# Kernel optimization log

Hardware: AMD Instinct MI355X
Metric: run time of the kernel (lower is better)

## Reference

```python
import jax, jax.numpy as jnp
import numpy as np

N_NODES = 50000
N_EDGES = 800000
IN_F = 96
HID = 64
N_CLS = 32


def setup_inputs() -> dict:
    key = jax.random.key(0)
    k1, k2, k3, k4 = jax.random.split(key, 4)
    x = jax.random.normal(k1, (N_NODES, IN_F), dtype=jnp.float32)
    edge_index = jax.random.randint(k2, (2, N_EDGES), 0, N_NODES, dtype=jnp.int64)
    # xavier_uniform init for weights, zeros for bias
    lim1 = float(np.sqrt(6.0 / (IN_F + HID)))
    lim2 = float(np.sqrt(6.0 / (HID + N_CLS)))
    W1 = jax.random.uniform(k3, (IN_F, HID), minval=-lim1, maxval=lim1, dtype=jnp.float32)
    W2 = jax.random.uniform(k4, (HID, N_CLS), minval=-lim2, maxval=lim2, dtype=jnp.float32)
    b1 = jnp.zeros((HID,), dtype=jnp.float32)
    b2 = jnp.zeros((N_CLS,), dtype=jnp.float32)
    return {"x": x, "edge_index": edge_index, "W1": W1, "b1": b1, "W2": W2, "b2": b2}


def _ghost_conv(h, src, dst, W, b, num_nodes):
    # gather neighbor feats per edge, per-edge matmul, scatter-add, bias
    msg = h[src] @ W                                   # [E, out]
    agg = jax.ops.segment_sum(msg, dst, num_segments=num_nodes)  # [N, out]
    return agg + b


def reference(x, edge_index, W1, b1, W2, b2):
    src, dst = edge_index[0], edge_index[1]
    n = x.shape[0]
    h = jax.nn.relu(_ghost_conv(x, src, dst, W1, b1, n))
    # F.dropout(training=False) is identity in eval mode
    out = _ghost_conv(h, src, dst, W2, b2, n)
    return jax.nn.log_softmax(out, axis=1)
```

## Files before the change

kernel.cpp:

```cpp
#include <hip/hip_runtime.h>
#include <hip/hip_bf16.h>
#include <hip/hip_fp8.h>

typedef __attribute__((ext_vector_type(8))) short bf16x8;
typedef __attribute__((ext_vector_type(4))) float f32x4;
typedef __attribute__((ext_vector_type(2))) float f32x2;

#define NBLK 256
#define NBINS_PAD 800
#define BCAP 2048
#define W1LD 104
#define HLD 72

__device__ inline unsigned short f2bf(float f) {
    unsigned u = __float_as_uint(f);
    return (unsigned short)((u + 0x7fffu + ((u >> 16) & 1u)) >> 16);
}
__device__ inline unsigned pack2(float a, float b) {
    return (unsigned)f2bf(a) | ((unsigned)f2bf(b) << 16);
}
__device__ inline float blo(unsigned u) { return __uint_as_float(u << 16); }
__device__ inline float bhi(unsigned u) { return __uint_as_float(u & 0xffff0000u); }

__device__ inline void acc8(float* a, uint4 v) {
    a[0] += blo(v.x); a[1] += bhi(v.x);
    a[2] += blo(v.y); a[3] += bhi(v.y);
    a[4] += blo(v.z); a[5] += bhi(v.z);
    a[6] += blo(v.w); a[7] += bhi(v.w);
}

__device__ inline void accf8x4(float* a, unsigned u) {
    f32x2 lo = __builtin_amdgcn_cvt_pk_f32_fp8((int)u, false);
    f32x2 hi = __builtin_amdgcn_cvt_pk_f32_fp8((int)u, true);
    a[0] += lo.x; a[1] += lo.y; a[2] += hi.x; a[3] += hi.y;
}
__device__ inline void accf8(float* a, uint4 v) {
    accf8x4(a, v.x); accf8x4(a + 4, v.y); accf8x4(a + 8, v.z); accf8x4(a + 12, v.w);
}

__global__ __launch_bounds__(256) void fused_hist_gemm1(
        const int* __restrict__ ei, int* __restrict__ counts, int E, int chunk, int nb,
        const float* __restrict__ W1, const float* __restrict__ W2,
        unsigned short* __restrict__ w2t,
        const float* __restrict__ X,
        unsigned char* __restrict__ y1f8, int Mtiles) {
    __shared__ int hist[NBINS_PAD];
    __shared__ unsigned short w1l[64 * W1LD];
    int b = blockIdx.x, t = threadIdx.x;
    if (b < NBLK) {
        for (int i = t; i < NBINS_PAD; i += 256) hist[i] = 0;
        __syncthreads();
        int e0 = b * chunk;
        int n = E - e0; if (n > chunk) n = chunk; if (n < 0) n = 0;
        for (int i = t; i < n; i += 256) atomicAdd(&hist[ei[E + e0 + i] >> 6], 1);
        __syncthreads();
        for (int j = t; j < nb; j += 256) counts[j * NBLK + b] = hist[j];
        return;
    }
    if (b == NBLK) {
        for (int idx = t; idx < 64 * 32; idx += 256) {
            int n = idx / 64, k = idx - n * 64;
            w2t[idx] = f2bf(W2[k * 32 + n]);
        }
        return;
    }
    for (int idx = t; idx < 96 * 64; idx += 256) {
        int n = idx / 96, k = idx - n * 96;
        w1l[n * W1LD + k] = f2bf(W1[k * 64 + n]);
    }
    __syncthreads();
    int wave = (b - NBLK - 1) * 4 + (t >> 6);
    if (wave >= Mtiles) return;
    int lane = t & 63;
    int l15 = lane & 15, quad = lane >> 4;
    const float* arow = X + (long)(wave * 16 + l15) * 96 + quad * 8;
    f32x4 acc[4] = {{0,0,0,0},{0,0,0,0},{0,0,0,0},{0,0,0,0}};
#pragma unroll
    for (int tt = 0; tt < 3; ++tt) {
        float4 p0 = *(const float4*)(arow + tt * 32);
        float4 p1 = *(const float4*)(arow + tt * 32 + 4);
        union { bf16x8 v; unsigned u[4]; } a;
        a.u[0] = pack2(p0.x, p0.y); a.u[1] = pack2(p0.z, p0.w);
        a.u[2] = pack2(p1.x, p1.y); a.u[3] = pack2(p1.z, p1.w);
#pragma unroll
        for (int nt = 0; nt < 4; ++nt) {
            bf16x8 bfr = *(const bf16x8*)(w1l + (nt * 16 + l15) * W1LD + tt * 32 + quad * 8);
            acc[nt] = __builtin_amdgcn_mfma_f32_16x16x32_bf16(a.v, bfr, acc[nt], 0, 0, 0);
        }
    }
    int mbase = wave * 16 + quad * 4;
#pragma unroll
    for (int nt = 0; nt < 4; ++nt) {
        int col = nt * 16 + l15;
        int pk = __builtin_amdgcn_cvt_pk_fp8_f32(acc[nt][0], acc[nt][1], 0, false);
        pk = __builtin_amdgcn_cvt_pk_fp8_f32(acc[nt][2], acc[nt][3], pk, true);
#pragma unroll
        for (int r = 0; r < 4; ++r)
            y1f8[(long)(mbase + r) * 64 + col] = (unsigned char)((pk >> (8 * r)) & 0xff);
    }
}

__global__ __launch_bounds__(256) void rowscan(int* __restrict__ counts,
                                               int* __restrict__ btot, int nb) {
    int w = (blockIdx.x * 256 + threadIdx.x) >> 6;
    int lane = threadIdx.x & 63;
    if (w >= nb) return;
    int* row = counts + (size_t)w * NBLK;
    int c0 = row[lane * 4], c1 = row[lane * 4 + 1];
    int c2 = row[lane * 4 + 2], c3 = row[lane * 4 + 3];
    int sum = c0 + c1 + c2 + c3;
    int s = sum;
#pragma unroll
    for (int o = 1; o < 64; o <<= 1) {
        int tt = __shfl_up(s, o);
        if (lane >= o) s += tt;
    }
    int run = s - sum;
    row[lane * 4] = run;     run += c0;
    row[lane * 4 + 1] = run; run += c1;
    row[lane * 4 + 2] = run; run += c2;
    row[lane * 4 + 3] = run;
    if (lane == 63) btot[w] = s;
}

__global__ __launch_bounds__(256) void blk_place(const int* __restrict__ ei,
                                                 const int* __restrict__ counts,
                                                 unsigned* __restrict__ pairs,
                                                 int E, int chunk, int nb) {
    __shared__ int cur[NBINS_PAD];
    int b = blockIdx.x, t = threadIdx.x;
    for (int j = t; j < nb; j += 256) cur[j] = (j << 11) + counts[j * NBLK + b];
    __syncthreads();
    int e0 = b * chunk;
    int n = E - e0; if (n > chunk) n = chunk; if (n < 0) n = 0;
    for (int i = t; i < n; i += 256) {
        int s = ei[e0 + i], d = ei[E + e0 + i];
        int j = d >> 6;
        int pos = atomicAdd(&cur[j], 1);
        if (pos < ((j + 1) << 11))
            pairs[pos] = (unsigned)s | ((unsigned)(d & 63) << 16);
    }
}

__global__ __launch_bounds__(256) void bucket_fused(
        const unsigned* __restrict__ pairs, const int* __restrict__ btot,
        const uint4* __restrict__ y1f8,
        const float* __restrict__ b1, const unsigned short* __restrict__ w2t,
        int2* __restrict__ noderange, int* __restrict__ srcs,
        unsigned short* __restrict__ y2, int N) {
    __shared__ unsigned spk[BCAP];
    __shared__ int lsrc[BCAP];
    __shared__ int cnt64[64], cur64[64], rs[64], re[64];
    __shared__ unsigned short htile[64 * HLD];
    int b = blockIdx.x, t = threadIdx.x;
    int base = b << 11;
    int cnt = btot[b]; if (cnt > BCAP) cnt = BCAP;
    if (t < 64) cnt64[t] = 0;
    __syncthreads();
    for (int i = t; i < cnt; i += 256) {
        unsigned p = pairs[base + i];
        spk[i] = p;
        atomicAdd(&cnt64[(p >> 16) & 63], 1);
    }
    __syncthreads();
    if (t < 64) {
        int v = cnt64[t], x = v;
#pragma unroll
        for (int o = 1; o < 64; o <<= 1) {
            int y = __shfl_up(x, o);
            if (t >= o) x += y;
        }
        int excl = x - v;
        cur64[t] = excl;
        rs[t] = excl;
        re[t] = excl + v;
        int node = b * 64 + t;
        if (node < N) noderange[node] = make_int2(base + excl, base + excl + v);
    }
    __syncthreads();
    for (int i = t; i < cnt; i += 256) {
        unsigned p = spk[i];
        int pos = atomicAdd(&cur64[(p >> 16) & 63], 1);
        lsrc[pos] = (int)(p & 0xffffu);
    }
    __syncthreads();
    for (int i = t; i < cnt; i += 256) srcs[base + i] = lsrc[i];

    int dl = t >> 2, q = t & 3;
    int s0 = rs[dl], s1 = re[dl];
    float a[16];
#pragma unroll
    for (int i = 0; i < 16; ++i) a[i] = 0.f;
    const uint4* ybase = y1f8 + q;
    int e = s0;
    for (; e + 8 <= s1; e += 8) {
        uint4 u0 = ybase[(long)lsrc[e] * 4],     u1 = ybase[(long)lsrc[e + 1] * 4];
        uint4 u2 = ybase[(long)lsrc[e + 2] * 4], u3 = ybase[(long)lsrc[e + 3] * 4];
        uint4 u4 = ybase[(long)lsrc[e + 4] * 4], u5 = ybase[(long)lsrc[e + 5] * 4];
        uint4 u6 = ybase[(long)lsrc[e + 6] * 4], u7 = ybase[(long)lsrc[e + 7] * 4];
        accf8(a, u0); accf8(a, u1); accf8(a, u2); accf8(a, u3);
        accf8(a, u4); accf8(a, u5); accf8(a, u6); accf8(a, u7);
    }
    for (; e < s1; ++e) accf8(a, ybase[(long)lsrc[e] * 4]);
    {
        const float* bq = b1 + q * 16;
        float v[16];
#pragma unroll
        for (int j = 0; j < 16; ++j) v[j] = fmaxf(a[j] + bq[j], 0.f);
        uint4 o0, o1;
        o0.x = pack2(v[0], v[1]);   o0.y = pack2(v[2], v[3]);
        o0.z = pack2(v[4], v[5]);   o0.w = pack2(v[6], v[7]);
        o1.x = pack2(v[8], v[9]);   o1.y = pack2(v[10], v[11]);
        o1.z = pack2(v[12], v[13]); o1.w = pack2(v[14], v[15]);
        uint4* hp = (uint4*)(htile + dl * HLD + q * 16);
        hp[0] = o0;
        hp[1] = o1;
    }
    __syncthreads();
    int w = t >> 6, lane = t & 63;
    int l15 = lane & 15, quad = lane >> 4;
    const unsigned short* arow = htile + (w * 16 + l15) * HLD + quad * 8;
    f32x4 acc2[2] = {{0,0,0,0},{0,0,0,0}};
#pragma unroll
    for (int t2 = 0; t2 < 2; ++t2) {
        bf16x8 af = *(const bf16x8*)(arow + t2 * 32);
#pragma unroll
        for (int nt = 0; nt < 2; ++nt) {
            bf16x8 bfr = *(const bf16x8*)(w2t + (long)(nt * 16 + l15) * 64 + t2 * 32 + quad * 8);
            acc2[nt] = __builtin_amdgcn_mfma_f32_16x16x32_bf16(af, bfr, acc2[nt], 0, 0, 0);
        }
    }
    int mbase = b * 64 + w * 16 + quad * 4;
#pragma unroll
    for (int nt = 0; nt < 2; ++nt) {
        int col = nt * 16 + l15;
#pragma unroll
        for (int r = 0; r < 4; ++r) {
            int n = mbase + r;
            if (n < N) y2[(long)n * 32 + col] = f2bf(acc2[nt][r]);
        }
    }
}

__global__ void gather_lsm(const uint4* __restrict__ y2, const int2* __restrict__ rng,
                           const int* __restrict__ srcs, const float* __restrict__ bias,
                           float* __restrict__ out, int N) {
    int gid = blockIdx.x * blockDim.x + threadIdx.x;
    int n = gid >> 2;
    if (n >= N) return;
    int q = gid & 3;
    int2 r01 = rng[n];
    int s0 = r01.x, s1 = r01.y;
    float a[8];
#pragma unroll
    for (int i = 0; i < 8; ++i) a[i] = 0.f;
    const uint4* base = y2 + q;
    int e = s0;
    for (; e + 8 <= s1; e += 8) {
        uint4 u0 = base[(long)srcs[e] * 4],     u1 = base[(long)srcs[e + 1] * 4];
        uint4 u2 = base[(long)srcs[e + 2] * 4], u3 = base[(long)srcs[e + 3] * 4];
        uint4 u4 = base[(long)srcs[e + 4] * 4], u5 = base[(long)srcs[e + 5] * 4];
        uint4 u6 = base[(long)srcs[e + 6] * 4], u7 = base[(long)srcs[e + 7] * 4];
        acc8(a, u0); acc8(a, u1); acc8(a, u2); acc8(a, u3);
        acc8(a, u4); acc8(a, u5); acc8(a, u6); acc8(a, u7);
    }
    for (; e < s1; ++e) acc8(a, base[(long)srcs[e] * 4]);
    const float* bq = bias + q * 8;
    float m = -1e30f;
#pragma unroll
    for (int i = 0; i < 8; ++i) { a[i] += bq[i]; m = fmaxf(m, a[i]); }
    m = fmaxf(m, __shfl_xor(m, 1));
    m = fmaxf(m, __shfl_xor(m, 2));
    float s = 0.f;
#pragma unroll
    for (int i = 0; i < 8; ++i) s += __expf(a[i] - m);
    s += __shfl_xor(s, 1);
    s += __shfl_xor(s, 2);
    float ls = m + __logf(s);
    float* op = out + (long)n * 32 + q * 8;
#pragma unroll
    for (int i = 0; i < 8; ++i) op[i] = a[i] - ls;
}

extern "C" void kernel_launch(void* const* d_in, const int* in_sizes, int n_in,
                              void* d_out, int out_size, void* d_ws, size_t ws_size,
                              hipStream_t stream) {
    const float* x  = (const float*)d_in[0];
    const int*   ei = (const int*)d_in[1];
    const float* W1 = (const float*)d_in[2];
    const float* b1 = (const float*)d_in[3];
    const float* W2 = (const float*)d_in[4];
    const float* b2 = (const float*)d_in[5];
    float* out = (float*)d_out;

    const int N = in_sizes[0] / 96;
    const int E = in_sizes[1] / 2;
    const int nb = (N + 63) / 64;
    const int chunk = (E + NBLK - 1) / NBLK;

    char* p = (char*)d_ws;
    unsigned char*  y1f8 = (unsigned char*)p;     p += (size_t)N * 64;
    unsigned short* y2   = (unsigned short*)p;    p += (size_t)N * 32 * 2;
    unsigned short* w2t  = (unsigned short*)p;    p += 64 * 32 * 2;
    int2* noderange = (int2*)p;                   p += (size_t)N * 8;
    int* counts = (int*)p;                        p += ((size_t)nb * NBLK * 4 + 12) & ~15ull;
    int* btot   = (int*)p;                        p += ((size_t)nb * 4 + 12) & ~15ull;
    unsigned* pairs = (unsigned*)p;               p += (size_t)nb * BCAP * 4;
    int* srcs   = (int*)p;                        p += (size_t)nb * BCAP * 4;

    const int Mtiles = N / 16;
    const int gblocks = (Mtiles + 3) / 4;

    fused_hist_gemm1<<<NBLK + 1 + gblocks, 256, 0, stream>>>(
        ei, counts, E, chunk, nb, W1, W2, w2t, x, y1f8, Mtiles);
    rowscan<<<(nb * 64 + 255) / 256, 256, 0, stream>>>(counts, btot, nb);
    blk_place<<<NBLK, 256, 0, stream>>>(ei, counts, pairs, E, chunk, nb);
    bucket_fused<<<nb, 256, 0, stream>>>(pairs, btot, (const uint4*)y1f8,
                                         b1, w2t, noderange, srcs, y2, N);
    gather_lsm<<<(N * 4 + 255) / 256, 256, 0, stream>>>(
        (const uint4*)y2, noderange, srcs, b2, out, N);
}
```

Measured before the change: 138.4 us.

## Fuse histogram and placement via global atomics, widen per-node gather parallelism

```diff
diff --git a/kernel.cpp b/kernel.cpp
--- a/kernel.cpp
+++ b/kernel.cpp
@@ -6,11 +6,12 @@
 typedef __attribute__((ext_vector_type(4))) float f32x4;
 typedef __attribute__((ext_vector_type(2))) float f32x2;
 
-#define NBLK 256
+#define NBLK 512
 #define NBINS_PAD 800
 #define BCAP 2048
 #define W1LD 104
 #define HLD 72
+#define GSTRIDE 16
 
 __device__ inline unsigned short f2bf(float f) {
     unsigned u = __float_as_uint(f);
@@ -38,13 +39,14 @@
     accf8x4(a, v.x); accf8x4(a + 4, v.y); accf8x4(a + 8, v.z); accf8x4(a + 12, v.w);
 }
 
-__global__ __launch_bounds__(256) void fused_hist_gemm1(
-        const int* __restrict__ ei, int* __restrict__ counts, int E, int chunk, int nb,
+__global__ __launch_bounds__(256, 5) void fused_front(
+        const int* __restrict__ ei, int* __restrict__ gcount, int E, int chunk, int nb,
         const float* __restrict__ W1, const float* __restrict__ W2,
         unsigned short* __restrict__ w2t,
         const float* __restrict__ X,
-        unsigned char* __restrict__ y1f8, int Mtiles) {
+        unsigned char* __restrict__ y1f8, unsigned* __restrict__ pairs, int Mtiles) {
     __shared__ int hist[NBINS_PAD];
+    __shared__ int cur[NBINS_PAD];
     __shared__ unsigned short w1l[64 * W1LD];
     int b = blockIdx.x, t = threadIdx.x;
     if (b < NBLK) {
@@ -52,21 +54,36 @@
         __syncthreads();
         int e0 = b * chunk;
         int n = E - e0; if (n > chunk) n = chunk; if (n < 0) n = 0;
-        for (int i = t; i < n; i += 256) atomicAdd(&hist[ei[E + e0 + i] >> 6], 1);
+        const int* dstp = ei + E + e0;
+        for (int i = t; i < n; i += 256) atomicAdd(&hist[dstp[i] >> 6], 1);
         __syncthreads();
-        for (int j = t; j < nb; j += 256) counts[j * NBLK + b] = hist[j];
+        for (int j = t; j < nb; j += 256) {
+            int c = hist[j];
+            int bs = j << 11;
+            if (c) bs += atomicAdd(&gcount[j * GSTRIDE], c);
+            cur[j] = bs;
+        }
+        __syncthreads();
+        const int* srcp = ei + e0;
+        for (int i = t; i < n; i += 256) {
+            int s = srcp[i], d = dstp[i];
+            int j = d >> 6;
+            int pos = atomicAdd(&cur[j], 1);
+            if (pos < ((j + 1) << 11))
+                pairs[pos] = (unsigned)s | ((unsigned)(d & 63) << 16);
+        }
         return;
     }
     if (b == NBLK) {
         for (int idx = t; idx < 64 * 32; idx += 256) {
-            int n = idx / 64, k = idx - n * 64;
-            w2t[idx] = f2bf(W2[k * 32 + n]);
+            int n2 = idx / 64, k = idx - n2 * 64;
+            w2t[idx] = f2bf(W2[k * 32 + n2]);
         }
         return;
     }
     for (int idx = t; idx < 96 * 64; idx += 256) {
-        int n = idx / 96, k = idx - n * 96;
-        w1l[n * W1LD + k] = f2bf(W1[k * 64 + n]);
+        int n2 = idx / 96, k = idx - n2 * 96;
+        w1l[n2 * W1LD + k] = f2bf(W1[k * 64 + n2]);
     }
     __syncthreads();
     int wave = (b - NBLK - 1) * 4 + (t >> 6);
@@ -100,50 +117,8 @@
     }
 }
 
-__global__ __launch_bounds__(256) void rowscan(int* __restrict__ counts,
-                                               int* __restrict__ btot, int nb) {
-    int w = (blockIdx.x * 256 + threadIdx.x) >> 6;
-    int lane = threadIdx.x & 63;
-    if (w >= nb) return;
-    int* row = counts + (size_t)w * NBLK;
-    int c0 = row[lane * 4], c1 = row[lane * 4 + 1];
-    int c2 = row[lane * 4 + 2], c3 = row[lane * 4 + 3];
-    int sum = c0 + c1 + c2 + c3;
-    int s = sum;
-#pragma unroll
-    for (int o = 1; o < 64; o <<= 1) {
-        int tt = __shfl_up(s, o);
-        if (lane >= o) s += tt;
-    }
-    int run = s - sum;
-    row[lane * 4] = run;     run += c0;
-    row[lane * 4 + 1] = run; run += c1;
-    row[lane * 4 + 2] = run; run += c2;
-    row[lane * 4 + 3] = run;
-    if (lane == 63) btot[w] = s;
-}
-
-__global__ __launch_bounds__(256) void blk_place(const int* __restrict__ ei,
-                                                 const int* __restrict__ counts,
-                                                 unsigned* __restrict__ pairs,
-                                                 int E, int chunk, int nb) {
-    __shared__ int cur[NBINS_PAD];
-    int b = blockIdx.x, t = threadIdx.x;
-    for (int j = t; j < nb; j += 256) cur[j] = (j << 11) + counts[j * NBLK + b];
-    __syncthreads();
-    int e0 = b * chunk;
-    int n = E - e0; if (n > chunk) n = chunk; if (n < 0) n = 0;
-    for (int i = t; i < n; i += 256) {
-        int s = ei[e0 + i], d = ei[E + e0 + i];
-        int j = d >> 6;
-        int pos = atomicAdd(&cur[j], 1);
-        if (pos < ((j + 1) << 11))
-            pairs[pos] = (unsigned)s | ((unsigned)(d & 63) << 16);
-    }
-}
-
-__global__ __launch_bounds__(256) void bucket_fused(
-        const unsigned* __restrict__ pairs, const int* __restrict__ btot,
+__global__ __launch_bounds__(1024) void bucket_fused(
+        const unsigned* __restrict__ pairs, const int* __restrict__ gcount,
         const uint4* __restrict__ y1f8,
         const float* __restrict__ b1, const unsigned short* __restrict__ w2t,
         int2* __restrict__ noderange, int* __restrict__ srcs,
@@ -154,10 +129,10 @@
     __shared__ unsigned short htile[64 * HLD];
     int b = blockIdx.x, t = threadIdx.x;
     int base = b << 11;
-    int cnt = btot[b]; if (cnt > BCAP) cnt = BCAP;
+    int cnt = gcount[b * GSTRIDE]; if (cnt > BCAP) cnt = BCAP;
     if (t < 64) cnt64[t] = 0;
     __syncthreads();
-    for (int i = t; i < cnt; i += 256) {
+    for (int i = t; i < cnt; i += 1024) {
         unsigned p = pairs[base + i];
         spk[i] = p;
         atomicAdd(&cnt64[(p >> 16) & 63], 1);
@@ -178,31 +153,34 @@
         if (node < N) noderange[node] = make_int2(base + excl, base + excl + v);
     }
     __syncthreads();
-    for (int i = t; i < cnt; i += 256) {
+    for (int i = t; i < cnt; i += 1024) {
         unsigned p = spk[i];
         int pos = atomicAdd(&cur64[(p >> 16) & 63], 1);
         lsrc[pos] = (int)(p & 0xffffu);
     }
     __syncthreads();
-    for (int i = t; i < cnt; i += 256) srcs[base + i] = lsrc[i];
-
-    int dl = t >> 2, q = t & 3;
-    int s0 = rs[dl], s1 = re[dl];
+    for (int i = t; i < cnt; i += 1024) srcs[base + i] = lsrc[i];
+
+    int dl = t >> 4, sub = t & 15, q = sub & 3, half = sub >> 2;
+    int s0 = rs[dl] + half, s1 = re[dl];
     float a[16];
 #pragma unroll
     for (int i = 0; i < 16; ++i) a[i] = 0.f;
     const uint4* ybase = y1f8 + q;
     int e = s0;
-    for (; e + 8 <= s1; e += 8) {
-        uint4 u0 = ybase[(long)lsrc[e] * 4],     u1 = ybase[(long)lsrc[e + 1] * 4];
-        uint4 u2 = ybase[(long)lsrc[e + 2] * 4], u3 = ybase[(long)lsrc[e + 3] * 4];
-        uint4 u4 = ybase[(long)lsrc[e + 4] * 4], u5 = ybase[(long)lsrc[e + 5] * 4];
-        uint4 u6 = ybase[(long)lsrc[e + 6] * 4], u7 = ybase[(long)lsrc[e + 7] * 4];
+    for (; e + 13 <= s1; e += 16) {
+        uint4 u0 = ybase[(long)lsrc[e] * 4];
+        uint4 u1 = ybase[(long)lsrc[e + 4] * 4];
+        uint4 u2 = ybase[(long)lsrc[e + 8] * 4];
+        uint4 u3 = ybase[(long)lsrc[e + 12] * 4];
         accf8(a, u0); accf8(a, u1); accf8(a, u2); accf8(a, u3);
-        accf8(a, u4); accf8(a, u5); accf8(a, u6); accf8(a, u7);
-    }
-    for (; e < s1; ++e) accf8(a, ybase[(long)lsrc[e] * 4]);
-    {
+    }
+    for (; e < s1; e += 4) accf8(a, ybase[(long)lsrc[e] * 4]);
+#pragma unroll
+    for (int i = 0; i < 16; ++i) a[i] += __shfl_xor(a[i], 4);
+#pragma unroll
+    for (int i = 0; i < 16; ++i) a[i] += __shfl_xor(a[i], 8);
+    if (half == 0) {
         const float* bq = b1 + q * 16;
         float v[16];
 #pragma unroll
@@ -217,54 +195,61 @@
         hp[1] = o1;
     }
     __syncthreads();
-    int w = t >> 6, lane = t & 63;
-    int l15 = lane & 15, quad = lane >> 4;
-    const unsigned short* arow = htile + (w * 16 + l15) * HLD + quad * 8;
-    f32x4 acc2[2] = {{0,0,0,0},{0,0,0,0}};
-#pragma unroll
-    for (int t2 = 0; t2 < 2; ++t2) {
-        bf16x8 af = *(const bf16x8*)(arow + t2 * 32);
+    int w = t >> 6;
+    if (w < 4) {
+        int lane = t & 63;
+        int l15 = lane & 15, quad = lane >> 4;
+        const unsigned short* arow = htile + (w * 16 + l15) * HLD + quad * 8;
+        f32x4 acc2[2] = {{0,0,0,0},{0,0,0,0}};
+#pragma unroll
+        for (int t2 = 0; t2 < 2; ++t2) {
+            bf16x8 af = *(const bf16x8*)(arow + t2 * 32);
+#pragma unroll
+            for (int nt = 0; nt < 2; ++nt) {
+                bf16x8 bfr = *(const bf16x8*)(w2t + (long)(nt * 16 + l15) * 64 + t2 * 32 + quad * 8);
+                acc2[nt] = __builtin_amdgcn_mfma_f32_16x16x32_bf16(af, bfr, acc2[nt], 0, 0, 0);
+            }
+        }
+        int mbase = b * 64 + w * 16 + quad * 4;
 #pragma unroll
         for (int nt = 0; nt < 2; ++nt) {
-            bf16x8 bfr = *(const bf16x8*)(w2t + (long)(nt * 16 + l15) * 64 + t2 * 32 + quad * 8);
-            acc2[nt] = __builtin_amdgcn_mfma_f32_16x16x32_bf16(af, bfr, acc2[nt], 0, 0, 0);
-        }
-    }
-    int mbase = b * 64 + w * 16 + quad * 4;
-#pragma unroll
-    for (int nt = 0; nt < 2; ++nt) {
-        int col = nt * 16 + l15;
-#pragma unroll
-        for (int r = 0; r < 4; ++r) {
-            int n = mbase + r;
-            if (n < N) y2[(long)n * 32 + col] = f2bf(acc2[nt][r]);
-        }
-    }
-}
-
-__global__ void gather_lsm(const uint4* __restrict__ y2, const int2* __restrict__ rng,
-                           const int* __restrict__ srcs, const float* __restrict__ bias,
-                           float* __restrict__ out, int N) {
+            int col = nt * 16 + l15;
+#pragma unroll
+            for (int r = 0; r < 4; ++r) {
+                int n = mbase + r;
+                if (n < N) y2[(long)n * 32 + col] = f2bf(acc2[nt][r]);
+            }
+        }
+    }
+}
+
+__global__ __launch_bounds__(256) void gather_lsm(
+        const uint4* __restrict__ y2, const int2* __restrict__ rng,
+        const int* __restrict__ srcs, const float* __restrict__ bias,
+        float* __restrict__ out, int N) {
     int gid = blockIdx.x * blockDim.x + threadIdx.x;
-    int n = gid >> 2;
+    int n = gid >> 4;
     if (n >= N) return;
-    int q = gid & 3;
+    int sub = gid & 15, q = sub & 3, half = sub >> 2;
     int2 r01 = rng[n];
-    int s0 = r01.x, s1 = r01.y;
+    int s0 = r01.x + half, s1 = r01.y;
     float a[8];
 #pragma unroll
     for (int i = 0; i < 8; ++i) a[i] = 0.f;
     const uint4* base = y2 + q;
     int e = s0;
-    for (; e + 8 <= s1; e += 8) {
-        uint4 u0 = base[(long)srcs[e] * 4],     u1 = base[(long)srcs[e + 1] * 4];
-        uint4 u2 = base[(long)srcs[e + 2] * 4], u3 = base[(long)srcs[e + 3] * 4];
-        uint4 u4 = base[(long)srcs[e + 4] * 4], u5 = base[(long)srcs[e + 5] * 4];
-        uint4 u6 = base[(long)srcs[e + 6] * 4], u7 = base[(long)srcs[e + 7] * 4];
+    for (; e + 13 <= s1; e += 16) {
+        uint4 u0 = base[(long)srcs[e] * 4];
+        uint4 u1 = base[(long)srcs[e + 4] * 4];
+        uint4 u2 = base[(long)srcs[e + 8] * 4];
+        uint4 u3 = base[(long)srcs[e + 12] * 4];
         acc8(a, u0); acc8(a, u1); acc8(a, u2); acc8(a, u3);
-        acc8(a, u4); acc8(a, u5); acc8(a, u6); acc8(a, u7);
-    }
-    for (; e < s1; ++e) acc8(a, base[(long)srcs[e] * 4]);
+    }
+    for (; e < s1; e += 4) acc8(a, base[(long)srcs[e] * 4]);
+#pragma unroll
+    for (int i = 0; i < 8; ++i) a[i] += __shfl_xor(a[i], 4);
+#pragma unroll
+    for (int i = 0; i < 8; ++i) a[i] += __shfl_xor(a[i], 8);
     const float* bq = bias + q * 8;
     float m = -1e30f;
 #pragma unroll
@@ -277,9 +262,13 @@
     s += __shfl_xor(s, 1);
     s += __shfl_xor(s, 2);
     float ls = m + __logf(s);
-    float* op = out + (long)n * 32 + q * 8;
-#pragma unroll
-    for (int i = 0; i < 8; ++i) op[i] = a[i] - ls;
+    if (half == 0) {
+        float* op = out + (long)n * 32 + q * 8;
+        float4 o0 = make_float4(a[0] - ls, a[1] - ls, a[2] - ls, a[3] - ls);
+        float4 o1 = make_float4(a[4] - ls, a[5] - ls, a[6] - ls, a[7] - ls);
+        *(float4*)op = o0;
+        *((float4*)op + 1) = o1;
+    }
 }
 
 extern "C" void kernel_launch(void* const* d_in, const int* in_sizes, int n_in,
@@ -303,20 +292,18 @@
     unsigned short* y2   = (unsigned short*)p;    p += (size_t)N * 32 * 2;
     unsigned short* w2t  = (unsigned short*)p;    p += 64 * 32 * 2;
     int2* noderange = (int2*)p;                   p += (size_t)N * 8;
-    int* counts = (int*)p;                        p += ((size_t)nb * NBLK * 4 + 12) & ~15ull;
-    int* btot   = (int*)p;                        p += ((size_t)nb * 4 + 12) & ~15ull;
+    int* gcount = (int*)p;                        p += (size_t)nb * GSTRIDE * 4;
     unsigned* pairs = (unsigned*)p;               p += (size_t)nb * BCAP * 4;
     int* srcs   = (int*)p;                        p += (size_t)nb * BCAP * 4;
 
     const int Mtiles = N / 16;
     const int gblocks = (Mtiles + 3) / 4;
 
-    fused_hist_gemm1<<<NBLK + 1 + gblocks, 256, 0, stream>>>(
-        ei, counts, E, chunk, nb, W1, W2, w2t, x, y1f8, Mtiles);
-    rowscan<<<(nb * 64 + 255) / 256, 256, 0, stream>>>(counts, btot, nb);
-    blk_place<<<NBLK, 256, 0, stream>>>(ei, counts, pairs, E, chunk, nb);
-    bucket_fused<<<nb, 256, 0, stream>>>(pairs, btot, (const uint4*)y1f8,
-                                         b1, w2t, noderange, srcs, y2, N);
-    gather_lsm<<<(N * 4 + 255) / 256, 256, 0, stream>>>(
+    hipMemsetAsync(gcount, 0, (size_t)nb * GSTRIDE * 4, stream);
+    fused_front<<<NBLK + 1 + gblocks, 256, 0, stream>>>(
+        ei, gcount, E, chunk, nb, W1, W2, w2t, x, y1f8, pairs, Mtiles);
+    bucket_fused<<<nb, 1024, 0, stream>>>(pairs, gcount, (const uint4*)y1f8,
+                                          b1, w2t, noderange, srcs, y2, N);
+    gather_lsm<<<(N * 16 + 255) / 256, 256, 0, stream>>>(
         (const uint4*)y2, noderange, srcs, b2, out, N);
 }
```

Measured after the change: 157.2 us. +13.6%, slower.
